# Kernel tuning notes

Measured on AMD Instinct MI355X. Metric: run time of the kernel, lower is better.

The kernel has to match this reference:

```python
import jax, jax.numpy as jnp
import numpy as np


def setup_inputs() -> dict:
    B, K, E, M, H, T, V = 32, 64, 512, 512, 512, 20, 32000
    key = jax.random.key(0)
    ks = jax.random.split(key, 8)
    s = 0.02
    return {
        "encoder_outputs": jax.random.normal(ks[0], (B, K, E), jnp.float32),
        "embedding_table": jax.random.normal(ks[1], (V, M), jnp.float32) * s,
        "Wa": jax.random.normal(ks[2], (2 * H + E, 1), jnp.float32) * s,
        "ba": jnp.zeros((1,), jnp.float32),
        "W_ih": jax.random.normal(ks[3], (4 * H, E + M), jnp.float32) * s,
        "W_hh": jax.random.normal(ks[4], (4 * H, H), jnp.float32) * s,
        "b_ih": jnp.zeros((4 * H,), jnp.float32),
        "b_hh": jnp.zeros((4 * H,), jnp.float32),
        "Wl": jax.random.normal(ks[5], (V, 2 * H + E + M), jnp.float32) * s,
        "bl": jnp.zeros((V,), jnp.float32),
        "captions": jax.random.randint(ks[6], (B, T), 0, V),
        "use_teacher_forcing": 1,
    }


def reference(encoder_outputs, embedding_table, Wa, ba, W_ih, W_hh, b_ih, b_hh,
              Wl, bl, captions, use_teacher_forcing):
    B, K, E = encoder_outputs.shape
    H = W_hh.shape[1]
    tf = bool(use_teacher_forcing)  # static python flag

    # h0 = c0 = last encoder output (requires E == H, as in the source)
    h0 = encoder_outputs[:, -1, :]
    c0 = h0

    caps_seq = captions.T  # (T, B); captions[:, i] becomes next token after step i

    def step(carry, cap_t):
        h, c, token = carry
        emb = embedding_table[token]                       # (B, M), dropout=0
        flat_state = jnp.concatenate([h, c], axis=-1)      # (B, 2H)
        # Bahdanau alignment over all K encoder steps at once
        al_in = jnp.concatenate(
            [jnp.broadcast_to(flat_state[:, None, :], (B, K, 2 * H)),
             encoder_outputs], axis=-1)                    # (B, K, 2H+E)
        scores = jnp.tanh(al_in @ Wa + ba)[..., 0]         # (B, K)
        attn = jax.nn.softmax(scores, axis=1)
        context = jnp.einsum('bk,bke->be', attn, encoder_outputs)  # (B, E)
        x = jnp.concatenate([context, emb], axis=-1)       # (B, E+M) == rnn_input
        # single LSTM step, PyTorch gate order i,f,g,o
        gates = x @ W_ih.T + b_ih + h @ W_hh.T + b_hh
        i_g, f_g, g_g, o_g = jnp.split(gates, 4, axis=-1)
        c_new = jax.nn.sigmoid(f_g) * c + jax.nn.sigmoid(i_g) * jnp.tanh(g_g)
        h_new = jax.nn.sigmoid(o_g) * jnp.tanh(c_new)
        # NOTE: source concatenates the PRE-update state here (faithful)
        final_input = jnp.concatenate([flat_state, x], axis=-1)  # (B, 2H+E+M)
        logp = jax.nn.log_softmax(final_input @ Wl.T + bl, axis=1)  # (B, V)
        next_token = cap_t if tf else jnp.argmax(logp, axis=1)
        return (h_new, c_new, next_token), logp

    init = (h0, c0, captions[:, 0])
    _, probs = jax.lax.scan(step, init, caps_seq)
    return jnp.transpose(probs, (1, 0, 2))  # (B, T, V)
```

## Files before the change

kernel.cpp:

```cpp
#include <hip/hip_runtime.h>
#include <hip/hip_bf16.h>
#include <stdint.h>

#define B_   32
#define K_   64
#define E_   512
#define H_   512
#define M_   512
#define T_   20
#define V_   32000
#define KIN  2048
#define NBLK 32

typedef __bf16 bf16x8 __attribute__((ext_vector_type(8)));
typedef float  f32x4  __attribute__((ext_vector_type(4)));

__device__ inline unsigned short f2bf_rne(float f) {
  union { float f; unsigned u; } v; v.f = f;
  unsigned r = v.u + 0x7FFFu + ((v.u >> 16) & 1u);
  return (unsigned short)(r >> 16);
}
__device__ inline float bf2f(unsigned short s) {
  union { unsigned u; float f; } v; v.u = ((unsigned)s) << 16;
  return v.f;
}
__device__ inline float sigm(float x) { return 1.f / (1.f + expf(-x)); }
__device__ inline unsigned ordf(float f) {
  unsigned u = __float_as_uint(f);
  return (u & 0x80000000u) ? ~u : (u | 0x80000000u);
}
__device__ __forceinline__ void gload16(const void* g, void* l) {
  __builtin_amdgcn_global_load_lds(
      (const __attribute__((address_space(1))) void*)g,
      (__attribute__((address_space(3))) void*)l, 16, 0, 0);
}


__global__ void k_prep(const float* __restrict__ W_ih, const float* __restrict__ W_hh,
                       const float* __restrict__ b_ih, const float* __restrict__ b_hh,
                       const float* __restrict__ enc, const float* __restrict__ embt,
                       const int* __restrict__ captions,
                       unsigned short* __restrict__ wih_hi, unsigned short* __restrict__ wih_lo,
                       unsigned short* __restrict__ whh_hi, unsigned short* __restrict__ whh_lo,
                       unsigned short* __restrict__ enc_bf, unsigned short* __restrict__ emb_bf,
                       float* __restrict__ bias_arr, float* __restrict__ score_part,
                       unsigned long long* __restrict__ argkey) {
  int tid0 = blockIdx.x * 256 + threadIdx.x;
  int NT = gridDim.x * 256;
  for (int i = tid0; i < 2048 * 1024; i += NT) {
    float f = W_ih[i];
    unsigned short h = f2bf_rne(f);
    wih_hi[i] = h; wih_lo[i] = f2bf_rne(f - bf2f(h));
  }
  for (int i = tid0; i < NBLK * 64 * 512; i += NT) {
    int e = i & 511, jj = (i >> 9) & 63, blk = i >> 15;
    int jg = (jj >> 4) * 512 + blk * 16 + (jj & 15);
    float f = W_hh[jg * 512 + e];
    unsigned short h = f2bf_rne(f);
    whh_hi[i] = h; whh_lo[i] = f2bf_rne(f - bf2f(h));
  }
  for (int i = tid0; i < 2048 * 512; i += NT) enc_bf[i] = f2bf_rne(enc[i]);
  for (int i = tid0; i < 640 * 512; i += NT) {
    int n = i >> 9, m = i & 511;
    int t = n >> 5, b = n & 31;
    int tok = captions[b * T_ + (t > 0 ? t - 1 : 0)];
    emb_bf[i] = f2bf_rne(embt[(size_t)tok * 512 + m]);
  }
  for (int i = tid0; i < 2048; i += NT) {
    int blk = i >> 6, jj = i & 63;
    int jg = (jj >> 4) * 512 + blk * 16 + (jj & 15);
    bias_arr[i] = b_ih[jg] + b_hh[jg];
  }
  for (int i = tid0; i < (T_ + 1) * 1024; i += NT) score_part[i] = 0.f;
  for (int i = tid0; i < 32; i += NT) argkey[i] = 0ull;
}

__global__ void k_init(const float* __restrict__ enc, const float* __restrict__ Wa,
                       float* __restrict__ hb, float* __restrict__ cb,
                       unsigned short* __restrict__ Fall,
                       float* __restrict__ enc_score, float* __restrict__ score_part) {
  int idx = blockIdx.x * 256 + threadIdx.x;
  int b = idx >> 9, i = idx & 511;
  float v = enc[(size_t)b * K_ * E_ + (size_t)(K_ - 1) * E_ + i];
  hb[b * H_ + i] = v;
  cb[b * H_ + i] = v;
  unsigned short bv = f2bf_rne(v);
  Fall[b * KIN + i] = bv;
  Fall[b * KIN + H_ + i] = bv;
  if (idx < B_ * K_) {
    int bb = idx >> 6, k = idx & 63;
    const float4* e4  = (const float4*)(enc + ((size_t)bb * K_ + k) * E_);
    const float4* wa4 = (const float4*)(Wa + 2 * H_);
    float acc = 0.f;
    #pragma unroll 4
    for (int q = 0; q < E_ / 4; ++q) {
      float4 a = e4[q], w = wa4[q];
      acc += a.x * w.x + a.y * w.y + a.z * w.z + a.w * w.w;
    }
    enc_score[idx] = acc;
  }
  if (idx < 2048) {
    int bb = idx >> 6, l = idx & 63;
    float s = 0.f;
    #pragma unroll
    for (int q = 0; q < 8; ++q) {
      int ii = l * 8 + q;
      float hv = enc[(size_t)bb * K_ * E_ + (size_t)(K_ - 1) * E_ + ii];
      s += hv * (Wa[ii] + Wa[512 + ii]);
    }
    for (int o = 32; o; o >>= 1) s += __shfl_down(s, o);
    if (l == 0) score_part[bb] = s;
  }
}

__global__ __launch_bounds__(256) void k_gpre(
    const unsigned short* __restrict__ whi, const unsigned short* __restrict__ wlo,
    int koff, const unsigned short* __restrict__ Bm,
    float* __restrict__ outp, int N) {
  int blk = blockIdx.x, nt = blockIdx.y;
  int tid = threadIdx.x;
  int l = tid & 63, w = tid >> 6, lv = l & 15, lg = l >> 4;
  const int n0 = nt * 128 + w * 32;

  f32x4 acc[4][2];
  #pragma unroll
  for (int jf = 0; jf < 4; ++jf)
    #pragma unroll
    for (int nf = 0; nf < 2; ++nf) acc[jf][nf] = (f32x4){0.f, 0.f, 0.f, 0.f};

  #pragma unroll 4
  for (int kk = 0; kk < 16; ++kk) {
    bf16x8 bfr[2];
    #pragma unroll
    for (int nf = 0; nf < 2; ++nf)
      bfr[nf] = *(const bf16x8*)(Bm + (size_t)(n0 + nf * 16 + lv) * 512 + kk * 32 + lg * 8);
    #pragma unroll
    for (int jf = 0; jf < 4; ++jf) {
      int jg = jf * 512 + blk * 16 + lv;
      bf16x8 ahi = *(const bf16x8*)(whi + (size_t)jg * 1024 + koff + kk * 32 + lg * 8);
      bf16x8 alo = *(const bf16x8*)(wlo + (size_t)jg * 1024 + koff + kk * 32 + lg * 8);
      #pragma unroll
      for (int nf = 0; nf < 2; ++nf) {
        acc[jf][nf] = __builtin_amdgcn_mfma_f32_16x16x32_bf16(ahi, bfr[nf], acc[jf][nf], 0, 0, 0);
        acc[jf][nf] = __builtin_amdgcn_mfma_f32_16x16x32_bf16(alo, bfr[nf], acc[jf][nf], 0, 0, 0);
      }
    }
  }
  #pragma unroll
  for (int jf = 0; jf < 4; ++jf)
    #pragma unroll
    for (int nf = 0; nf < 2; ++nf)
      #pragma unroll
      for (int jr = 0; jr < 4; ++jr) {
        int n = n0 + nf * 16 + lv;
        int jj = jf * 16 + 4 * lg + jr;
        outp[((size_t)blk * N + n) * 64 + jj] = acc[jf][nf][jr];
      }
}

__global__ __launch_bounds__(256) void k_step(
    const float* __restrict__ enc, const float* __restrict__ embt,
    const float* __restrict__ Wa, const float* __restrict__ ba,
    const float* __restrict__ W_ih, const float* __restrict__ W_hh,
    const float* __restrict__ b_ih, const float* __restrict__ b_hh,
    const float* __restrict__ Wl, const float* __restrict__ bl,
    const int* __restrict__ captions, const int* __restrict__ tf_flag,
    const float* __restrict__ Genc, const float* __restrict__ Gemb,
    const unsigned short* __restrict__ whh_hi, const unsigned short* __restrict__ whh_lo,
    const float* __restrict__ bias_arr, const float* __restrict__ enc_score,
    float* __restrict__ score_part, float* __restrict__ attn_w,
    unsigned short* __restrict__ Fall, float* __restrict__ hb, float* __restrict__ cb,
    unsigned long long* __restrict__ argkey, int t) {
  const int blk = blockIdx.x;
  const int tid = threadIdx.x;
  __shared__ float attn_s[B_ * K_];
  __shared__ float gsA[64 * 33];
  __shared__ float scC[512];
  __shared__ float score_t[32];
  const float* cbc = cb + (t & 1) * B_ * H_;
  float* cbn = cb + ((t + 1) & 1) * B_ * H_;

  if (tf_flag[0]) {
    if (tid < 32) {
      float s = 0.f;
      #pragma unroll 8
      for (int p = 0; p < 32; ++p) s += score_part[t * 1024 + p * 32 + tid];
      score_t[tid] = s;
    }
    __syncthreads();
    {
      int w = tid >> 6, l = tid & 63;
      float ba0 = ba[0];
      for (int bb = 0; bb < 8; ++bb) {
        int b = w * 8 + bb;
        float s = tanhf(score_t[b] + enc_score[b * 64 + l] + ba0);
        float m = s;
        for (int o = 32; o; o >>= 1) m = fmaxf(m, __shfl_xor(m, o));
        float e = expf(s - m);
        float sum = e;
        for (int o = 32; o; o >>= 1) sum += __shfl_xor(sum, o);
        float a = e / sum;
        attn_s[b * 64 + l] = a;
        if (b == blk) attn_w[(t * 32 + b) * 64 + l] = a;
      }
    }
    __syncthreads();
    {
      const f32x4* G4 = (const f32x4*)Genc;
      const f32x4* E4 = (const f32x4*)Gemb;
      const f32x4* B4 = (const f32x4*)bias_arr;
      #pragma unroll
      for (int rr = 0; rr < 2; ++rr) {
        int idx = rr * 256 + tid;
        int b = idx >> 4, jj4 = idx & 15;
        const f32x4* gp = G4 + ((size_t)blk * 2048 + b * 64) * 16 + jj4;
        const float* ap = attn_s + b * 64;
        f32x4 s = {0.f, 0.f, 0.f, 0.f};
        #pragma unroll 8
        for (int k = 0; k < 64; ++k) {
          float a = ap[k];
          f32x4 g = gp[(size_t)k * 16];
          s[0] += a * g[0]; s[1] += a * g[1]; s[2] += a * g[2]; s[3] += a * g[3];
        }
        f32x4 e = E4[((size_t)blk * 640 + t * 32 + b) * 16 + jj4];
        f32x4 bb = B4[blk * 16 + jj4];
        #pragma unroll
        for (int q = 0; q < 4; ++q) {
          float v = s[q] + (e[q] + bb[q]);
          gsA[(jj4 * 4 + q) * 33 + b] = v;
        }
      }
    }
    __syncthreads();
    {
      int g = tid >> 6, l = tid & 63, lv = l & 15, lg = l >> 4;
      const unsigned short* ah = whh_hi + ((size_t)blk * 64 + g * 16 + lv) * 512 + lg * 8;
      const unsigned short* al = whh_lo + ((size_t)blk * 64 + g * 16 + lv) * 512 + lg * 8;
      const unsigned short* f0 = Fall + ((size_t)t * 32 + lv) * KIN + lg * 8;
      const unsigned short* f1 = Fall + ((size_t)t * 32 + 16 + lv) * KIN + lg * 8;
      f32x4 a0 = {0.f, 0.f, 0.f, 0.f};
      f32x4 a1 = {0.f, 0.f, 0.f, 0.f};
      #pragma unroll 8
      for (int kk = 0; kk < 16; ++kk) {
        bf16x8 hi = *(const bf16x8*)(ah + kk * 32);
        bf16x8 lo = *(const bf16x8*)(al + kk * 32);
        bf16x8 b0 = *(const bf16x8*)(f0 + kk * 32);
        bf16x8 b1 = *(const bf16x8*)(f1 + kk * 32);
        a0 = __builtin_amdgcn_mfma_f32_16x16x32_bf16(hi, b0, a0, 0, 0, 0);
        a0 = __builtin_amdgcn_mfma_f32_16x16x32_bf16(lo, b0, a0, 0, 0, 0);
        a1 = __builtin_amdgcn_mfma_f32_16x16x32_bf16(hi, b1, a1, 0, 0, 0);
        a1 = __builtin_amdgcn_mfma_f32_16x16x32_bf16(lo, b1, a1, 0, 0, 0);
      }
      #pragma unroll
      for (int jr = 0; jr < 4; ++jr) {
        int jj = g * 16 + 4 * lg + jr;
        gsA[jj * 33 + lv]      += a0[jr];
        gsA[jj * 33 + 16 + lv] += a1[jr];
      }
    }
    __syncthreads();
    #pragma unroll
    for (int rr = 0; rr < 2; ++rr) {
      int idx = tid + rr * 256;
      int b = idx & 31, r = idx >> 5;
      int ii = blk * 16 + r;
      float ig = gsA[(r) * 33 + b];
      float fg = gsA[(16 + r) * 33 + b];
      float gg = gsA[(32 + r) * 33 + b];
      float og = gsA[(48 + r) * 33 + b];
      float cv = cbc[b * H_ + ii];
      float cn = sigm(fg) * cv + sigm(ig) * tanhf(gg);
      float hn = sigm(og) * tanhf(cn);
      cbn[b * H_ + ii] = cn;
      Fall[((size_t)(t + 1) * 32 + b) * KIN + ii] = f2bf_rne(hn);
      Fall[((size_t)(t + 1) * 32 + b) * KIN + H_ + ii] = f2bf_rne(cn);
      scC[r * 32 + b] = hn * Wa[ii] + cn * Wa[512 + ii];
    }
    __syncthreads();
    if (tid < 32) {
      float s = 0.f;
      #pragma unroll
      for (int r = 0; r < 16; ++r) s += scC[r * 32 + tid];
      score_part[(t + 1) * 1024 + blk * 32 + tid] = s;
    }
  } else {
    const int b = blk;
    __shared__ float xls[KIN];
    __shared__ float gls[2048];
    __shared__ int tok_s;
    __shared__ unsigned long long bred[256];
    const float* hbc = hb + (t & 1) * B_ * H_;
    float* hbn = hb + ((t + 1) & 1) * B_ * H_;
    if (tid == 0) {
      float s = 0.f;
      for (int p = 0; p < 32; ++p) s += score_part[t * 1024 + p * 32 + b];
      score_t[0] = s;
      tok_s = (t == 0) ? captions[b * T_]
                       : (int)(0xFFFFFFFFu - (unsigned)(argkey[b] & 0xFFFFFFFFull));
    }
    __syncthreads();
    if (tid < 64) {
      float s = tanhf(score_t[0] + enc_score[b * 64 + tid] + ba[0]);
      float m = s;
      for (int o = 32; o; o >>= 1) m = fmaxf(m, __shfl_xor(m, o));
      float e = expf(s - m);
      float sum = e;
      for (int o = 32; o; o >>= 1) sum += __shfl_xor(sum, o);
      attn_s[tid] = e / sum;
    }
    __syncthreads();
    for (int i = tid; i < 512; i += 256) {
      xls[i] = hbc[b * H_ + i];
      xls[512 + i] = cbc[b * H_ + i];
      float a = 0.f;
      for (int k = 0; k < 64; ++k) a += attn_s[k] * enc[((size_t)b * 64 + k) * 512 + i];
      xls[1024 + i] = a;
      xls[1536 + i] = embt[(size_t)tok_s * 512 + i];
    }
    __syncthreads();
    for (int i = tid; i < 1024; i += 256)
      Fall[((size_t)t * 32 + b) * KIN + 1024 + i] = f2bf_rne(xls[1024 + i]);
    for (int j = tid; j < 2048; j += 256) {
      float a = b_ih[j] + b_hh[j];
      for (int e = 0; e < 1024; ++e) a += W_ih[(size_t)j * 1024 + e] * xls[1024 + e];
      for (int e = 0; e < 512; ++e)  a += W_hh[(size_t)j * 512 + e] * xls[e];
      gls[j] = a;
    }
    __syncthreads();
    {
      float sc = 0.f;
      for (int i = tid; i < 512; i += 256) {
        float ig = gls[i], fg = gls[512 + i], gg = gls[1024 + i], og = gls[1536 + i];
        float cv = xls[512 + i];
        float cn = sigm(fg) * cv + sigm(ig) * tanhf(gg);
        float hn = sigm(og) * tanhf(cn);
        hbn[b * H_ + i] = hn;
        cbn[b * H_ + i] = cn;
        Fall[((size_t)(t + 1) * 32 + b) * KIN + i] = f2bf_rne(hn);
        Fall[((size_t)(t + 1) * 32 + b) * KIN + H_ + i] = f2bf_rne(cn);
        sc += hn * Wa[i] + cn * Wa[512 + i];
      }
      scC[tid] = sc;
    }
    __syncthreads();
    if (tid == 0) {
      float s = 0.f;
      for (int q = 0; q < 256; ++q) s += scC[q];
      score_part[(t + 1) * 1024 + b] = s;
    }
    unsigned long long best = 0ull;
    for (int v = tid; v < V_; v += 256) {
      float d = bl[v];
      const float* wr = Wl + (size_t)v * KIN;
      for (int k = 0; k < KIN; ++k) d += wr[k] * xls[k];
      unsigned long long key = ((unsigned long long)ordf(d) << 32) | (0xFFFFFFFFu - (unsigned)v);
      if (key > best) best = key;
    }
    bred[tid] = best;
    __syncthreads();
    for (int o = 128; o; o >>= 1) {
      if (tid < o) bred[tid] = bred[tid] > bred[tid + o] ? bred[tid] : bred[tid + o];
      __syncthreads();
    }
    if (tid == 0) argkey[b] = bred[0];
  }
}

__global__ void k_fill(const float* __restrict__ enc, const unsigned short* __restrict__ emb_bf,
                       const float* __restrict__ attn_w, const int* __restrict__ tf_flag,
                       unsigned short* __restrict__ Fall) {
  if (tf_flag[0] == 0) return;
  int n = blockIdx.x;
  int b = n & 31;
  int tid = threadIdx.x;
  __shared__ float aw[64];
  if (tid < 64) aw[tid] = attn_w[n * 64 + tid];
  __syncthreads();
  for (int e = tid; e < 512; e += 256) {
    float a = 0.f;
    #pragma unroll 8
    for (int k = 0; k < 64; ++k) a += aw[k] * enc[((size_t)b * 64 + k) * 512 + e];
    Fall[(size_t)n * KIN + 1024 + e] = f2bf_rne(a);
  }
  for (int m = tid; m < 512; m += 256)
    Fall[(size_t)n * KIN + 1536 + m] = emb_bf[n * 512 + m];
}

__global__ void k_conv(const float* __restrict__ src, unsigned short* __restrict__ dst, int n4) {
  int i = blockIdx.x * blockDim.x + threadIdx.x;
  int stride = gridDim.x * blockDim.x;
  for (; i < n4; i += stride) {
    f32x4 v = __builtin_nontemporal_load((const f32x4*)src + i);
    ushort4 o;
    o.x = f2bf_rne(v.x); o.y = f2bf_rne(v.y); o.z = f2bf_rne(v.z); o.w = f2bf_rne(v.w);
    ((ushort4*)dst)[i] = o;
  }
}

#define GM   128
#define GNP  320
#define ABYTES 40960
#define BUFB  57344

__global__ __launch_bounds__(512, 2) void k_gemm(
    const unsigned short* __restrict__ wl_bf,
    const unsigned short* __restrict__ F,
    const float* __restrict__ bl,
    float* __restrict__ out) {
  extern __shared__ unsigned char lds[];
  const int tid = threadIdx.x;
  const int l = tid & 63, w = tid >> 6, lv = l & 15, lg = l >> 4;
  const int wm = w >> 2, wn = w & 3;
  const int m0 = blockIdx.x * GM;

  float blv[4];
  #pragma unroll
  for (int mi = 0; mi < 4; ++mi) blv[mi] = bl[m0 + wm * 64 + mi * 16 + lv];

  f32x4 acc[4][5];
  #pragma unroll
  for (int mi = 0; mi < 4; ++mi)
    #pragma unroll
    for (int ni = 0; ni < 5; ++ni) acc[mi][ni] = (f32x4){0.f, 0.f, 0.f, 0.f};

#define STAGE(c, buf) do {                                                    \
    int kb_ = ((c) & 31) * 64;                                                \
    int nb_ = ((c) >> 5) * GNP;                                               \
    unsigned char* bs_ = lds + (buf) * BUFB;                                  \
    _Pragma("unroll")                                                         \
    for (int i_ = 0; i_ < 5; ++i_) {                                          \
      int s_ = i_ * 512 + tid;                                                \
      int kq_ = s_ / 320, n_ = s_ - kq_ * 320;                                \
      gload16(F + (size_t)(nb_ + n_) * KIN + kb_ + kq_ * 8, bs_ + s_ * 16);   \
    }                                                                         \
    _Pragma("unroll")                                                         \
    for (int j_ = 0; j_ < 2; ++j_) {                                          \
      int s_ = j_ * 512 + tid;                                                \
      int kq_ = s_ >> 7, m_ = s_ & 127;                                       \
      gload16(wl_bf + (size_t)(m0 + m_) * KIN + kb_ + kq_ * 8,                \
              bs_ + ABYTES + s_ * 16);                                        \
    }                                                                         \
  } while (0)

#define COMPUTE(buf) do {                                                     \
    unsigned char* bs_ = lds + (buf) * BUFB;                                  \
    _Pragma("unroll")                                                         \
    for (int kk2_ = 0; kk2_ < 2; ++kk2_) {                                    \
      int kq_ = kk2_ * 4 + lg;                                                \
      bf16x8 bf_[4];                                                          \
      _Pragma("unroll")                                                       \
      for (int mi = 0; mi < 4; ++mi)                                          \
        bf_[mi] = *(const bf16x8*)(bs_ + ABYTES +                             \
                    (size_t)(kq_ * 128 + wm * 64 + mi * 16 + lv) * 16);       \
      _Pragma("unroll")                                                       \
      for (int ni = 0; ni < 5; ++ni) {                                        \
        bf16x8 af_ = *(const bf16x8*)(bs_ +                                   \
                    (size_t)(kq_ * 320 + wn * 80 + ni * 16 + lv) * 16);       \
        _Pragma("unroll")                                                     \
        for (int mi = 0; mi < 4; ++mi)                                        \
          acc[mi][ni] = __builtin_amdgcn_mfma_f32_16x16x32_bf16(              \
                          af_, bf_[mi], acc[mi][ni], 0, 0, 0);                \
      }                                                                       \
    }                                                                         \
  } while (0)

#define WRITEOUT(pass) do {                                                   \
    _Pragma("unroll")                                                         \
    for (int mi = 0; mi < 4; ++mi) {                                          \
      int v_ = m0 + wm * 64 + mi * 16 + lv;                                   \
      _Pragma("unroll")                                                       \
      for (int ni = 0; ni < 5; ++ni) {                                        \
        _Pragma("unroll")                                                     \
        for (int j_ = 0; j_ < 4; ++j_) {                                      \
          int n_ = (pass) * GNP + wn * 80 + ni * 16 + 4 * lg + j_;            \
          int tt_ = n_ >> 5, bb_ = n_ & 31;                                   \
          out[((size_t)bb_ * T_ + tt_) * V_ + v_] = acc[mi][ni][j_] + blv[mi];\
        }                                                                     \
      }                                                                       \
    }                                                                         \
  } while (0)

  STAGE(0, 0);
  int cur = 0;
  for (int c = 0; c < 64; ++c) {
    __syncthreads();
    if (c < 63) STAGE(c + 1, cur ^ 1);
    COMPUTE(cur);
    if (c == 31) {
      WRITEOUT(0);
      #pragma unroll
      for (int mi = 0; mi < 4; ++mi)
        #pragma unroll
        for (int ni = 0; ni < 5; ++ni) acc[mi][ni] = (f32x4){0.f, 0.f, 0.f, 0.f};
    }
    cur ^= 1;
  }
  WRITEOUT(1);
#undef STAGE
#undef COMPUTE
#undef WRITEOUT
}

__global__ void k_lsm(float* __restrict__ out) {
  float4* p = (float4*)(out + (size_t)blockIdx.x * V_);
  int tid = threadIdx.x;
  __shared__ float smax[4], ssum[4];
  const int N4 = V_ / 4;
  float m = -1e30f, s = 0.f;
  for (int i = tid; i < N4; i += 256) {
    float4 v = p[i];
    float lm = fmaxf(fmaxf(v.x, v.y), fmaxf(v.z, v.w));
    if (lm > m) { s *= expf(m - lm); m = lm; }
    s += expf(v.x - m) + expf(v.y - m) + expf(v.z - m) + expf(v.w - m);
  }
  for (int o = 32; o; o >>= 1) {
    float m2 = __shfl_xor(m, o), s2 = __shfl_xor(s, o);
    float mn = fmaxf(m, m2);
    s = s * expf(m - mn) + s2 * expf(m2 - mn);
    m = mn;
  }
  if ((tid & 63) == 0) { smax[tid >> 6] = m; ssum[tid >> 6] = s; }
  __syncthreads();
  float mg = fmaxf(fmaxf(smax[0], smax[1]), fmaxf(smax[2], smax[3]));
  float sg = ssum[0] * expf(smax[0] - mg) + ssum[1] * expf(smax[1] - mg)
           + ssum[2] * expf(smax[2] - mg) + ssum[3] * expf(smax[3] - mg);
  float lse = mg + logf(sg);
  for (int i = tid; i < N4; i += 256) {
    float4 v = p[i];
    v.x -= lse; v.y -= lse; v.z -= lse; v.w -= lse;
    p[i] = v;
  }
}

extern "C" void kernel_launch(void* const* d_in, const int* in_sizes, int n_in,
                              void* d_out, int out_size, void* d_ws, size_t ws_size,
                              hipStream_t stream) {
  const float* enc      = (const float*)d_in[0];
  const float* embt     = (const float*)d_in[1];
  const float* Wa       = (const float*)d_in[2];
  const float* ba       = (const float*)d_in[3];
  const float* W_ih     = (const float*)d_in[4];
  const float* W_hh     = (const float*)d_in[5];
  const float* b_ih     = (const float*)d_in[6];
  const float* b_hh     = (const float*)d_in[7];
  const float* Wl       = (const float*)d_in[8];
  const float* bl       = (const float*)d_in[9];
  const int*   captions = (const int*)d_in[10];
  const int*   tf       = (const int*)d_in[11];
  float* out = (float*)d_out;
  char*  ws  = (char*)d_ws;

  size_t off = 0;
  unsigned short* Fall = (unsigned short*)(ws + off); off += (size_t)(T_ + 1) * B_ * KIN * 2;
  float* hb            = (float*)(ws + off);          off += (size_t)2 * B_ * H_ * 4;
  float* cb            = (float*)(ws + off);          off += (size_t)2 * B_ * H_ * 4;
  float* enc_score     = (float*)(ws + off);          off += (size_t)B_ * K_ * 4;
  float* score_part    = (float*)(ws + off);          off += (size_t)(T_ + 1) * 1024 * 4;
  float* attn_w        = (float*)(ws + off);          off += (size_t)T_ * B_ * K_ * 4;
  unsigned long long* argkey = (unsigned long long*)(ws + off); off += 256;
  float* bias_arr      = (float*)(ws + off);          off += 2048 * 4;
  off = (off + 1023) & ~(size_t)1023;
  unsigned short* wih_hi = (unsigned short*)(ws + off); off += (size_t)2048 * 1024 * 2;
  unsigned short* wih_lo = (unsigned short*)(ws + off); off += (size_t)2048 * 1024 * 2;
  unsigned short* whh_hi = (unsigned short*)(ws + off); off += (size_t)NBLK * 64 * 512 * 2;
  unsigned short* whh_lo = (unsigned short*)(ws + off); off += (size_t)NBLK * 64 * 512 * 2;
  unsigned short* enc_bf = (unsigned short*)(ws + off); off += (size_t)2048 * 512 * 2;
  unsigned short* emb_bf = (unsigned short*)(ws + off); off += (size_t)640 * 512 * 2;
  float* Genc          = (float*)(ws + off);          off += (size_t)NBLK * 2048 * 64 * 4;
  float* Gemb          = (float*)(ws + off);          off += (size_t)NBLK * 640 * 64 * 4;
  unsigned short* wl_bf = (unsigned short*)(ws + off); off += (size_t)V_ * KIN * 2;

  k_prep<<<512, 256, 0, stream>>>(W_ih, W_hh, b_ih, b_hh, enc, embt, captions,
                                  wih_hi, wih_lo, whh_hi, whh_lo, enc_bf, emb_bf,
                                  bias_arr, score_part, argkey);
  k_init<<<64, 256, 0, stream>>>(enc, Wa, hb, cb, Fall, enc_score, score_part);
  k_gpre<<<dim3(NBLK, 16), 256, 0, stream>>>(wih_hi, wih_lo, 0, enc_bf, Genc, 2048);
  k_gpre<<<dim3(NBLK, 5), 256, 0, stream>>>(wih_hi, wih_lo, 512, emb_bf, Gemb, 640);

  for (int t = 0; t < T_; ++t) {
    k_step<<<NBLK, 256, 0, stream>>>(enc, embt, Wa, ba, W_ih, W_hh, b_ih, b_hh,
                                     Wl, bl, captions, tf, Genc, Gemb,
                                     whh_hi, whh_lo, bias_arr, enc_score,
                                     score_part, attn_w, Fall, hb, cb, argkey, t);
  }
  k_fill<<<T_ * B_, 256, 0, stream>>>(enc, emb_bf, attn_w, tf, Fall);
  k_conv<<<8192, 256, 0, stream>>>(Wl, wl_bf, V_ * KIN / 4);
  k_gemm<<<V_ / GM, 512, 2 * BUFB, stream>>>(wl_bf, Fall, bl, out);
  k_lsm<<<B_ * T_, 256, 0, stream>>>(out);
}
```

Baseline: 813.4 us.

## Overlap vocab projection with recurrent steps in a fused per-step kernel

Replaces the post-loop fill, convert and large GEMM kernels with a fused per-step launch. It has 32 recurrent blocks plus 250 extra blocks that compute the vocabulary projection for the previous timestep's features while the current step runs. The Wl bf16 conversion and the embedding copy into the feature buffer move into the prep kernel, and the context vector is written directly during the step. The aim is to hide the large output GEMM under the latency-bound recurrence, at the cost of a GEMV-style kernel with less weight reuse that rereads Wl every step, plus one extra launch and a 128KB LDS allocation per launch.

```diff
diff --git a/kernel.cpp b/kernel.cpp
--- a/kernel.cpp
+++ b/kernel.cpp
@@ -11,6 +11,7 @@
 #define V_   32000
 #define KIN  2048
 #define NBLK 32
+#define NGEMV 250
 
 typedef __bf16 bf16x8 __attribute__((ext_vector_type(8)));
 typedef float  f32x4  __attribute__((ext_vector_type(4)));
@@ -44,9 +45,17 @@
                        unsigned short* __restrict__ whh_hi, unsigned short* __restrict__ whh_lo,
                        unsigned short* __restrict__ enc_bf, unsigned short* __restrict__ emb_bf,
                        float* __restrict__ bias_arr, float* __restrict__ score_part,
-                       unsigned long long* __restrict__ argkey) {
+                       unsigned long long* __restrict__ argkey,
+                       const float* __restrict__ Wl, unsigned short* __restrict__ wl_bf,
+                       unsigned short* __restrict__ Fall) {
   int tid0 = blockIdx.x * 256 + threadIdx.x;
   int NT = gridDim.x * 256;
+  for (int i = tid0; i < V_ * KIN / 4; i += NT) {
+    f32x4 v = __builtin_nontemporal_load((const f32x4*)Wl + i);
+    ushort4 o;
+    o.x = f2bf_rne(v.x); o.y = f2bf_rne(v.y); o.z = f2bf_rne(v.z); o.w = f2bf_rne(v.w);
+    ((ushort4*)wl_bf)[i] = o;
+  }
   for (int i = tid0; i < 2048 * 1024; i += NT) {
     float f = W_ih[i];
     unsigned short h = f2bf_rne(f);
@@ -64,7 +73,9 @@
     int n = i >> 9, m = i & 511;
     int t = n >> 5, b = n & 31;
     int tok = captions[b * T_ + (t > 0 ? t - 1 : 0)];
-    emb_bf[i] = f2bf_rne(embt[(size_t)tok * 512 + m]);
+    unsigned short ev = f2bf_rne(embt[(size_t)tok * 512 + m]);
+    emb_bf[i] = ev;
+    Fall[(size_t)n * KIN + 1536 + m] = ev;
   }
   for (int i = tid0; i < 2048; i += NT) {
     int blk = i >> 6, jj = i & 63;
@@ -158,7 +169,7 @@
       }
 }
 
-__global__ __launch_bounds__(256) void k_step(
+__global__ __launch_bounds__(256) void k_fused(
     const float* __restrict__ enc, const float* __restrict__ embt,
     const float* __restrict__ Wa, const float* __restrict__ ba,
     const float* __restrict__ W_ih, const float* __restrict__ W_hh,
@@ -168,15 +179,74 @@
     const float* __restrict__ Genc, const float* __restrict__ Gemb,
     const unsigned short* __restrict__ whh_hi, const unsigned short* __restrict__ whh_lo,
     const float* __restrict__ bias_arr, const float* __restrict__ enc_score,
-    float* __restrict__ score_part, float* __restrict__ attn_w,
-    unsigned short* __restrict__ Fall, float* __restrict__ hb, float* __restrict__ cb,
-    unsigned long long* __restrict__ argkey, int t) {
+    float* __restrict__ score_part, unsigned short* __restrict__ Fall,
+    float* __restrict__ hb, float* __restrict__ cb,
+    unsigned long long* __restrict__ argkey,
+    const unsigned short* __restrict__ wl_bf, float* __restrict__ out, int t) {
+  extern __shared__ unsigned char smem[];
   const int blk = blockIdx.x;
   const int tid = threadIdx.x;
-  __shared__ float attn_s[B_ * K_];
-  __shared__ float gsA[64 * 33];
-  __shared__ float scC[512];
-  __shared__ float score_t[32];
+
+  if (blk >= NBLK) {
+    if (t == 0) return;
+    const int c = t - 1;
+    const unsigned short* Fc = Fall + (size_t)c * 32 * KIN;
+    unsigned char* Alds = smem;
+    int l = tid & 63, w = tid >> 6, lv = l & 15, lg = l >> 4;
+
+    #pragma unroll
+    for (int q = 0; q < 32; ++q) {
+      int i = w * 32 + q;
+      int row = i >> 2;
+      int phys = ((i & 3) << 6) + l;
+      int gslot = phys ^ (row & 15);
+      gload16(Fc + row * 2048 + gslot * 8, Alds + i * 1024);
+    }
+    __syncthreads();
+
+    int gb = blk - NBLK;
+    int v  = gb * 128 + w * 16 + lv;
+    const unsigned short* gB0 = wl_bf + (size_t)v * KIN + lg * 8;
+    const unsigned short* gB1 = wl_bf + (size_t)(v + 64) * KIN + lg * 8;
+    f32x4 a00 = {0.f, 0.f, 0.f, 0.f};
+    f32x4 a01 = {0.f, 0.f, 0.f, 0.f};
+    f32x4 a10 = {0.f, 0.f, 0.f, 0.f};
+    f32x4 a11 = {0.f, 0.f, 0.f, 0.f};
+
+    #pragma unroll 8
+    for (int kk = 0; kk < 64; ++kk) {
+      bf16x8 b0 = *(const bf16x8*)(gB0 + kk * 32);
+      bf16x8 b1 = *(const bf16x8*)(gB1 + kk * 32);
+      int ao_ = (((kk * 4) + lg) ^ lv) << 4;
+      bf16x8 f0 = *(const bf16x8*)(Alds + lv * 4096 + ao_);
+      bf16x8 f1 = *(const bf16x8*)(Alds + (16 + lv) * 4096 + ao_);
+      a00 = __builtin_amdgcn_mfma_f32_16x16x32_bf16(f0, b0, a00, 0, 0, 0);
+      a01 = __builtin_amdgcn_mfma_f32_16x16x32_bf16(f1, b0, a01, 0, 0, 0);
+      a10 = __builtin_amdgcn_mfma_f32_16x16x32_bf16(f0, b1, a10, 0, 0, 0);
+      a11 = __builtin_amdgcn_mfma_f32_16x16x32_bf16(f1, b1, a11, 0, 0, 0);
+    }
+
+    float blv0 = bl[v], blv1 = bl[v + 64];
+    int r0 = lg * 4;
+    #pragma unroll
+    for (int j = 0; j < 4; ++j) {
+      out[((size_t)(r0 + j) * T_ + c) * V_ + v]           = a00[j] + blv0;
+      out[((size_t)(16 + r0 + j) * T_ + c) * V_ + v]      = a01[j] + blv0;
+      out[((size_t)(r0 + j) * T_ + c) * V_ + v + 64]      = a10[j] + blv1;
+      out[((size_t)(16 + r0 + j) * T_ + c) * V_ + v + 64] = a11[j] + blv1;
+    }
+    return;
+  }
+
+  if (t >= T_) return;
+  float* attn_s  = (float*)smem;
+  float* gsA     = attn_s + 2048;
+  float* scC     = gsA + 2112;
+  float* score_t_ = scC + 512;
+  int*   token_sp = (int*)(score_t_ + 32);
+  float* xls     = (float*)(token_sp + 8);
+  float* gls     = xls + 2048;
+  unsigned long long* bred = (unsigned long long*)(gls + 2048);
   const float* cbc = cb + (t & 1) * B_ * H_;
   float* cbn = cb + ((t + 1) & 1) * B_ * H_;
 
@@ -185,7 +255,7 @@
       float s = 0.f;
       #pragma unroll 8
       for (int p = 0; p < 32; ++p) s += score_part[t * 1024 + p * 32 + tid];
-      score_t[tid] = s;
+      score_t_[tid] = s;
     }
     __syncthreads();
     {
@@ -193,15 +263,13 @@
       float ba0 = ba[0];
       for (int bb = 0; bb < 8; ++bb) {
         int b = w * 8 + bb;
-        float s = tanhf(score_t[b] + enc_score[b * 64 + l] + ba0);
+        float s = tanhf(score_t_[b] + enc_score[b * 64 + l] + ba0);
         float m = s;
         for (int o = 32; o; o >>= 1) m = fmaxf(m, __shfl_xor(m, o));
         float e = expf(s - m);
         float sum = e;
         for (int o = 32; o; o >>= 1) sum += __shfl_xor(sum, o);
-        float a = e / sum;
-        attn_s[b * 64 + l] = a;
-        if (b == blk) attn_w[(t * 32 + b) * 64 + l] = a;
+        attn_s[b * 64 + l] = e / sum;
       }
     }
     __syncthreads();
@@ -231,6 +299,15 @@
         }
       }
     }
+    {
+      const float* aw = attn_s + blk * 64;
+      for (int e = tid; e < 512; e += 256) {
+        float a = 0.f;
+        #pragma unroll 8
+        for (int k = 0; k < 64; ++k) a += aw[k] * enc[((size_t)blk * 64 + k) * 512 + e];
+        Fall[((size_t)t * 32 + blk) * KIN + 1024 + e] = f2bf_rne(a);
+      }
+    }
     __syncthreads();
     {
       int g = tid >> 6, l = tid & 63, lv = l & 15, lg = l >> 4;
@@ -285,22 +362,18 @@
     }
   } else {
     const int b = blk;
-    __shared__ float xls[KIN];
-    __shared__ float gls[2048];
-    __shared__ int tok_s;
-    __shared__ unsigned long long bred[256];
     const float* hbc = hb + (t & 1) * B_ * H_;
     float* hbn = hb + ((t + 1) & 1) * B_ * H_;
     if (tid == 0) {
       float s = 0.f;
       for (int p = 0; p < 32; ++p) s += score_part[t * 1024 + p * 32 + b];
-      score_t[0] = s;
-      tok_s = (t == 0) ? captions[b * T_]
-                       : (int)(0xFFFFFFFFu - (unsigned)(argkey[b] & 0xFFFFFFFFull));
+      score_t_[0] = s;
+      token_sp[0] = (t == 0) ? captions[b * T_]
+                             : (int)(0xFFFFFFFFu - (unsigned)(argkey[b] & 0xFFFFFFFFull));
     }
     __syncthreads();
     if (tid < 64) {
-      float s = tanhf(score_t[0] + enc_score[b * 64 + tid] + ba[0]);
+      float s = tanhf(score_t_[0] + enc_score[b * 64 + tid] + ba[0]);
       float m = s;
       for (int o = 32; o; o >>= 1) m = fmaxf(m, __shfl_xor(m, o));
       float e = expf(s - m);
@@ -315,7 +388,7 @@
       float a = 0.f;
       for (int k = 0; k < 64; ++k) a += attn_s[k] * enc[((size_t)b * 64 + k) * 512 + i];
       xls[1024 + i] = a;
-      xls[1536 + i] = embt[(size_t)tok_s * 512 + i];
+      xls[1536 + i] = embt[(size_t)token_sp[0] * 512 + i];
     }
     __syncthreads();
     for (int i = tid; i < 1024; i += 256)
@@ -364,141 +437,6 @@
     }
     if (tid == 0) argkey[b] = bred[0];
   }
-}
-
-__global__ void k_fill(const float* __restrict__ enc, const unsigned short* __restrict__ emb_bf,
-                       const float* __restrict__ attn_w, const int* __restrict__ tf_flag,
-                       unsigned short* __restrict__ Fall) {
-  if (tf_flag[0] == 0) return;
-  int n = blockIdx.x;
-  int b = n & 31;
-  int tid = threadIdx.x;
-  __shared__ float aw[64];
-  if (tid < 64) aw[tid] = attn_w[n * 64 + tid];
-  __syncthreads();
-  for (int e = tid; e < 512; e += 256) {
-    float a = 0.f;
-    #pragma unroll 8
-    for (int k = 0; k < 64; ++k) a += aw[k] * enc[((size_t)b * 64 + k) * 512 + e];
-    Fall[(size_t)n * KIN + 1024 + e] = f2bf_rne(a);
-  }
-  for (int m = tid; m < 512; m += 256)
-    Fall[(size_t)n * KIN + 1536 + m] = emb_bf[n * 512 + m];
-}
-
-__global__ void k_conv(const float* __restrict__ src, unsigned short* __restrict__ dst, int n4) {
-  int i = blockIdx.x * blockDim.x + threadIdx.x;
-  int stride = gridDim.x * blockDim.x;
-  for (; i < n4; i += stride) {
-    f32x4 v = __builtin_nontemporal_load((const f32x4*)src + i);
-    ushort4 o;
-    o.x = f2bf_rne(v.x); o.y = f2bf_rne(v.y); o.z = f2bf_rne(v.z); o.w = f2bf_rne(v.w);
-    ((ushort4*)dst)[i] = o;
-  }
-}
-
-#define GM   128
-#define GNP  320
-#define ABYTES 40960
-#define BUFB  57344
-
-__global__ __launch_bounds__(512, 2) void k_gemm(
-    const unsigned short* __restrict__ wl_bf,
-    const unsigned short* __restrict__ F,
-    const float* __restrict__ bl,
-    float* __restrict__ out) {
-  extern __shared__ unsigned char lds[];
-  const int tid = threadIdx.x;
-  const int l = tid & 63, w = tid >> 6, lv = l & 15, lg = l >> 4;
-  const int wm = w >> 2, wn = w & 3;
-  const int m0 = blockIdx.x * GM;
-
-  float blv[4];
-  #pragma unroll
-  for (int mi = 0; mi < 4; ++mi) blv[mi] = bl[m0 + wm * 64 + mi * 16 + lv];
-
-  f32x4 acc[4][5];
-  #pragma unroll
-  for (int mi = 0; mi < 4; ++mi)
-    #pragma unroll
-    for (int ni = 0; ni < 5; ++ni) acc[mi][ni] = (f32x4){0.f, 0.f, 0.f, 0.f};
-
-#define STAGE(c, buf) do {                                                    \
-    int kb_ = ((c) & 31) * 64;                                                \
-    int nb_ = ((c) >> 5) * GNP;                                               \
-    unsigned char* bs_ = lds + (buf) * BUFB;                                  \
-    _Pragma("unroll")                                                         \
-    for (int i_ = 0; i_ < 5; ++i_) {                                          \
-      int s_ = i_ * 512 + tid;                                                \
-      int kq_ = s_ / 320, n_ = s_ - kq_ * 320;                                \
-      gload16(F + (size_t)(nb_ + n_) * KIN + kb_ + kq_ * 8, bs_ + s_ * 16);   \
-    }                                                                         \
-    _Pragma("unroll")                                                         \
-    for (int j_ = 0; j_ < 2; ++j_) {                                          \
-      int s_ = j_ * 512 + tid;                                                \
-      int kq_ = s_ >> 7, m_ = s_ & 127;                                       \
-      gload16(wl_bf + (size_t)(m0 + m_) * KIN + kb_ + kq_ * 8,                \
-              bs_ + ABYTES + s_ * 16);                                        \
-    }                                                                         \
-  } while (0)
-
-#define COMPUTE(buf) do {                                                     \
-    unsigned char* bs_ = lds + (buf) * BUFB;                                  \
-    _Pragma("unroll")                                                         \
-    for (int kk2_ = 0; kk2_ < 2; ++kk2_) {                                    \
-      int kq_ = kk2_ * 4 + lg;                                                \
-      bf16x8 bf_[4];                                                          \
-      _Pragma("unroll")                                                       \
-      for (int mi = 0; mi < 4; ++mi)                                          \
-        bf_[mi] = *(const bf16x8*)(bs_ + ABYTES +                             \
-                    (size_t)(kq_ * 128 + wm * 64 + mi * 16 + lv) * 16);       \
-      _Pragma("unroll")                                                       \
-      for (int ni = 0; ni < 5; ++ni) {                                        \
-        bf16x8 af_ = *(const bf16x8*)(bs_ +                                   \
-                    (size_t)(kq_ * 320 + wn * 80 + ni * 16 + lv) * 16);       \
-        _Pragma("unroll")                                                     \
-        for (int mi = 0; mi < 4; ++mi)                                        \
-          acc[mi][ni] = __builtin_amdgcn_mfma_f32_16x16x32_bf16(              \
-                          af_, bf_[mi], acc[mi][ni], 0, 0, 0);                \
-      }                                                                       \
-    }                                                                         \
-  } while (0)
-
-#define WRITEOUT(pass) do {                                                   \
-    _Pragma("unroll")                                                         \
-    for (int mi = 0; mi < 4; ++mi) {                                          \
-      int v_ = m0 + wm * 64 + mi * 16 + lv;                                   \
-      _Pragma("unroll")                                                       \
-      for (int ni = 0; ni < 5; ++ni) {                                        \
-        _Pragma("unroll")                                                     \
-        for (int j_ = 0; j_ < 4; ++j_) {                                      \
-          int n_ = (pass) * GNP + wn * 80 + ni * 16 + 4 * lg + j_;            \
-          int tt_ = n_ >> 5, bb_ = n_ & 31;                                   \
-          out[((size_t)bb_ * T_ + tt_) * V_ + v_] = acc[mi][ni][j_] + blv[mi];\
-        }                                                                     \
-      }                                                                       \
-    }                                                                         \
-  } while (0)
-
-  STAGE(0, 0);
-  int cur = 0;
-  for (int c = 0; c < 64; ++c) {
-    __syncthreads();
-    if (c < 63) STAGE(c + 1, cur ^ 1);
-    COMPUTE(cur);
-    if (c == 31) {
-      WRITEOUT(0);
-      #pragma unroll
-      for (int mi = 0; mi < 4; ++mi)
-        #pragma unroll
-        for (int ni = 0; ni < 5; ++ni) acc[mi][ni] = (f32x4){0.f, 0.f, 0.f, 0.f};
-    }
-    cur ^= 1;
-  }
-  WRITEOUT(1);
-#undef STAGE
-#undef COMPUTE
-#undef WRITEOUT
 }
 
 __global__ void k_lsm(float* __restrict__ out) {
@@ -556,7 +494,6 @@
   float* cb            = (float*)(ws + off);          off += (size_t)2 * B_ * H_ * 4;
   float* enc_score     = (float*)(ws + off);          off += (size_t)B_ * K_ * 4;
   float* score_part    = (float*)(ws + off);          off += (size_t)(T_ + 1) * 1024 * 4;
-  float* attn_w        = (float*)(ws + off);          off += (size_t)T_ * B_ * K_ * 4;
   unsigned long long* argkey = (unsigned long long*)(ws + off); off += 256;
   float* bias_arr      = (float*)(ws + off);          off += 2048 * 4;
   off = (off + 1023) & ~(size_t)1023;
@@ -572,19 +509,16 @@
 
   k_prep<<<512, 256, 0, stream>>>(W_ih, W_hh, b_ih, b_hh, enc, embt, captions,
                                   wih_hi, wih_lo, whh_hi, whh_lo, enc_bf, emb_bf,
-                                  bias_arr, score_part, argkey);
+                                  bias_arr, score_part, argkey, Wl, wl_bf, Fall);
   k_init<<<64, 256, 0, stream>>>(enc, Wa, hb, cb, Fall, enc_score, score_part);
   k_gpre<<<dim3(NBLK, 16), 256, 0, stream>>>(wih_hi, wih_lo, 0, enc_bf, Genc, 2048);
   k_gpre<<<dim3(NBLK, 5), 256, 0, stream>>>(wih_hi, wih_lo, 512, emb_bf, Gemb, 640);
 
-  for (int t = 0; t < T_; ++t) {
-    k_step<<<NBLK, 256, 0, stream>>>(enc, embt, Wa, ba, W_ih, W_hh, b_ih, b_hh,
-                                     Wl, bl, captions, tf, Genc, Gemb,
-                                     whh_hi, whh_lo, bias_arr, enc_score,
-                                     score_part, attn_w, Fall, hb, cb, argkey, t);
-  }
-  k_fill<<<T_ * B_, 256, 0, stream>>>(enc, emb_bf, attn_w, tf, Fall);
-  k_conv<<<8192, 256, 0, stream>>>(Wl, wl_bf, V_ * KIN / 4);
-  k_gemm<<<V_ / GM, 512, 2 * BUFB, stream>>>(wl_bf, Fall, bl, out);
+  for (int t = 0; t <= T_; ++t) {
+    k_fused<<<NBLK + NGEMV, 256, 131072, stream>>>(
+        enc, embt, Wa, ba, W_ih, W_hh, b_ih, b_hh, Wl, bl, captions, tf,
+        Genc, Gemb, whh_hi, whh_lo, bias_arr, enc_score,
+        score_part, Fall, hb, cb, argkey, wl_bf, out, t);
+  }
   k_lsm<<<B_ * T_, 256, 0, stream>>>(out);
 }
```

Result: slower. 1.110 ms (+36.5%).
